# Kernel optimization log

Measured on AMD Instinct MI355X. Metric: run time of the kernel, lower is better.

## Reference

```python
import jax, jax.numpy as jnp
import numpy as np


def silu(x):
    return x * jax.nn.sigmoid(x)


def setup_inputs() -> dict:
    key = jax.random.key(0)
    ks = jax.random.split(key, 12)
    B, S, Dm = 2, 2048, 768
    I, N, R, K = 1536, 16, 48, 4
    s = 0.02
    return {
        "input_states": jax.random.normal(ks[0], (B, S, Dm), jnp.float32),
        "in_proj_w": jax.random.normal(ks[1], (2 * I, Dm), jnp.float32) * s,
        "conv_w": jax.random.normal(ks[2], (I, 1, K), jnp.float32) * s,
        "conv_b": jax.random.normal(ks[3], (I,), jnp.float32) * s,
        "x_proj_w": jax.random.normal(ks[4], (R + 2 * N, I), jnp.float32) * s,
        "dt_proj_w": jax.random.normal(ks[5], (I, R), jnp.float32) * s,
        "dt_proj_b": jax.random.normal(ks[6], (I,), jnp.float32) * s,
        "A_log": jax.random.normal(ks[7], (I, N), jnp.float32) * 0.5,
        "D": jax.random.normal(ks[8], (I,), jnp.float32) * s,
        "out_proj_w": jax.random.normal(ks[9], (Dm, I), jnp.float32) * s,
        "alpha": jax.random.uniform(ks[10], (I,), jnp.float32),
        "feature_gating": jax.random.uniform(ks[11], (I,), jnp.float32),
    }


def reference(input_states, in_proj_w, conv_w, conv_b, x_proj_w,
              dt_proj_w, dt_proj_b, A_log, D, out_proj_w,
              alpha, feature_gating):
    Bsz, S, _ = input_states.shape
    I, N = A_log.shape
    R = dt_proj_w.shape[1]
    K = conv_w.shape[-1]

    # in_proj (no bias), chunk into hidden / gate, each [B, I, S]
    proj = jnp.einsum('bsd,ed->bse', input_states, in_proj_w)  # [B, S, 2I]
    hidden, gate = jnp.split(proj.transpose(0, 2, 1), 2, axis=1)

    # causal depthwise conv1d + SiLU
    h = jax.lax.conv_general_dilated(
        hidden, conv_w, window_strides=(1,), padding=[(K - 1, 0)],
        dimension_numbers=('NCH', 'OIH', 'NCH'), feature_group_count=I)
    h = silu(h + conv_b[None, :, None])  # [B, I, S]

    # x_proj -> time_step, B, C
    ssm_p = jnp.einsum('bis,ei->bse', h, x_proj_w)  # [B, S, R+2N]
    ts, Bm, Cm = jnp.split(ssm_p, [R, R + N], axis=-1)

    dt = jax.nn.softplus(jnp.einsum('bsr,ir->bsi', ts, dt_proj_w) + dt_proj_b)
    dt = dt.transpose(0, 2, 1)                       # [B, I, S]
    dt = dt.at[:, :, -1].multiply(alpha[None, :])    # alpha scales last step

    A = -jnp.exp(A_log.astype(jnp.float32))          # [I, N]
    dA = jnp.exp(A[None, :, None, :] * dt[:, :, :, None])       # [B, I, S, N]
    dBu = dt[:, :, :, None] * Bm[:, None, :, :] * h[:, :, :, None]  # [B, I, S, N]

    def step(state, xs):
        dA_t, dBu_t, C_t = xs
        state = dA_t * state + dBu_t                 # [B, I, N]
        y = jnp.einsum('bin,bn->bi', state, C_t)
        return state, y

    init = jnp.zeros((Bsz, I, N), input_states.dtype)
    _, ys = jax.lax.scan(
        step, init,
        (dA.transpose(2, 0, 1, 3), dBu.transpose(2, 0, 1, 3), Cm.transpose(1, 0, 2)))
    y = ys.transpose(1, 2, 0)                        # [B, I, S]

    y = (y + h * D[None, :, None]) * silu(gate)
    y = y.at[:, :, -1].multiply(feature_gating[None, :])
    return jnp.einsum('bis,di->bsd', y, out_proj_w)  # [B, S, Dm]
```

## Files before the change

### kernel.cpp

```cpp
#include <hip/hip_runtime.h>
#include <math.h>


static constexpr int S_LEN  = 2048;
static constexpr int DMODEL = 768;
static constexpr int ICH    = 1536;
static constexpr int NST    = 16;
static constexpr int MROWS  = 4096;
static constexpr int NCH    = 64;
static constexpr int CHS    = 32;
static constexpr int CSTR   = 2 * ICH * NST;

typedef _Float16 f16;
typedef f16 f16x8 __attribute__((ext_vector_type(8)));
typedef f16 f16x4 __attribute__((ext_vector_type(4)));
typedef f16 f16x2 __attribute__((ext_vector_type(2)));
typedef float f32x4 __attribute__((ext_vector_type(4)));

#if __has_builtin(__builtin_amdgcn_exp2f)
#define EXP2F(x) __builtin_amdgcn_exp2f(x)
#else
#define EXP2F(x) exp2f(x)
#endif

typedef __attribute__((address_space(3))) void lds_void;
typedef const __attribute__((address_space(1))) void glb_void;

__device__ __forceinline__ void glds16(f16* l, const f16* g) {
    __builtin_amdgcn_global_load_lds((glb_void*)g, (lds_void*)l, 16, 0, 0);
}

__device__ __forceinline__ float silu_f(float x) {
    return x / (1.0f + __expf(-x));
}

__global__ __launch_bounds__(256) void cvt3(
    const float* __restrict__ s0, f16* __restrict__ d0, int n0,
    const float* __restrict__ s1, f16* __restrict__ d1, int n1,
    const float* __restrict__ s2, f16* __restrict__ d2)
{
    int i = (blockIdx.x * 256 + threadIdx.x) * 4;
    const float* s; f16* d;
    if (i < n0)            { s = s0 + i;            d = d0 + i; }
    else if (i < n0 + n1)  { s = s1 + (i - n0);     d = d1 + (i - n0); }
    else                   { s = s2 + (i - n0 - n1); d = d2 + (i - n0 - n1); }
    float4 v = *(const float4*)s;
    f16x4 o = { (f16)v.x, (f16)v.y, (f16)v.z, (f16)v.w };
    *(f16x4*)d = o;
}

__global__ __launch_bounds__(256) void k1m(
    const f16* __restrict__ Xh,
    const f16* __restrict__ Wh,
    f16* __restrict__ hidden,
    f16* __restrict__ sgate)
{
    __shared__ __align__(16) f16 As[2][128 * 32];
    __shared__ __align__(16) f16 Bs[2][64 * 32];
    const int tid = threadIdx.x;
    const int lane = tid & 63, wave = tid >> 6;
    const int quad = lane >> 4, l16 = lane & 15;
    const int wm = wave & 1, wn = wave >> 1;
    const int m0 = blockIdx.x * 128, n0 = blockIdx.y * 64;
    const int l_row = lane >> 2, l_c8 = (lane & 3) * 8;

    const f16* Ag = Xh + (size_t)(m0 + wave * 16 + l_row) * 768 + l_c8;
    const f16* Bg = Wh + (size_t)(n0 + wave * 16 + l_row) * 768 + l_c8;
    const int aLo = (wave * 16) * 32, aHi = (64 + wave * 16) * 32;
    const int bOff = (wave * 16) * 32;

#define K1_STAGE(buf, kk)                                        \
    do {                                                         \
        glds16(&As[buf][aLo], Ag + (kk));                        \
        glds16(&As[buf][aHi], Ag + (size_t)64 * 768 + (kk));     \
        glds16(&Bs[buf][bOff], Bg + (kk));                       \
    } while (0)

#define K1_COMPUTE(buf)                                                        \
    do {                                                                       \
        f16x8 af[4], bf[2];                                                    \
        _Pragma("unroll")                                                      \
        for (int mi = 0; mi < 4; ++mi)                                         \
            af[mi] = *(const f16x8*)&As[buf][(wm * 64 + mi * 16 + l16) * 32 + quad * 8]; \
        _Pragma("unroll")                                                      \
        for (int ni = 0; ni < 2; ++ni)                                         \
            bf[ni] = *(const f16x8*)&Bs[buf][(wn * 32 + ni * 16 + l16) * 32 + quad * 8]; \
        _Pragma("unroll")                                                      \
        for (int mi = 0; mi < 4; ++mi)                                         \
            _Pragma("unroll")                                                  \
            for (int ni = 0; ni < 2; ++ni)                                     \
                acc[mi][ni] = __builtin_amdgcn_mfma_f32_16x16x32_f16(          \
                    af[mi], bf[ni], acc[mi][ni], 0, 0, 0);                     \
    } while (0)

    K1_STAGE(0, 0);
    __syncthreads();

    f32x4 acc[4][2] = {};
    for (int k0 = 0; k0 < 768; k0 += 64) {
        K1_STAGE(1, k0 + 32);
        K1_COMPUTE(0);
        __syncthreads();
        if (k0 + 64 < 768) K1_STAGE(0, k0 + 64);
        K1_COMPUTE(1);
        __syncthreads();
    }
#undef K1_STAGE
#undef K1_COMPUTE

    const bool isGate = (n0 >= ICH);
    f16* outp = isGate ? sgate : hidden;
    const int e0 = (isGate ? (n0 - ICH) : n0) + wn * 32 + l16;
    #pragma unroll
    for (int mi = 0; mi < 4; ++mi) {
        #pragma unroll
        for (int ni = 0; ni < 2; ++ni) {
            #pragma unroll
            for (int r = 0; r < 4; ++r) {
                int m = m0 + wm * 64 + mi * 16 + quad * 4 + r;
                int e = e0 + ni * 16;
                float v = acc[mi][ni][r];
                if (isGate) v = silu_f(v);
                outp[(size_t)m * ICH + e] = (f16)v;
            }
        }
    }
}

__global__ __launch_bounds__(256) void k2_conv(
    const f16* __restrict__ hidden,
    const float* __restrict__ conv_w,
    const float* __restrict__ conv_b,
    f16* __restrict__ h)
{
    int idx = blockIdx.x * 256 + threadIdx.x;
    int i4 = idx % 384;
    int m  = idx / 384;
    int s  = m & (S_LEN - 1);
    const f16* base = hidden + (size_t)m * ICH + i4 * 4;
    const int c0 = i4 * 4;
    float4 wa = *(const float4*)(conv_w + (c0 + 0) * 4);
    float4 wb = *(const float4*)(conv_w + (c0 + 1) * 4);
    float4 wc = *(const float4*)(conv_w + (c0 + 2) * 4);
    float4 wd = *(const float4*)(conv_w + (c0 + 3) * 4);
    float4 bv = *(const float4*)(conv_b + c0);
    f16x4 z = {};
    f16x4 x0 = *(const f16x4*)(base);
    f16x4 x1 = (s >= 1) ? *(const f16x4*)(base - ICH)     : z;
    f16x4 x2 = (s >= 2) ? *(const f16x4*)(base - 2 * ICH) : z;
    f16x4 x3 = (s >= 3) ? *(const f16x4*)(base - 3 * ICH) : z;
    float r0 = bv.x + wa.x * (float)x3[0] + wa.y * (float)x2[0] + wa.z * (float)x1[0] + wa.w * (float)x0[0];
    float r1 = bv.y + wb.x * (float)x3[1] + wb.y * (float)x2[1] + wb.z * (float)x1[1] + wb.w * (float)x0[1];
    float r2 = bv.z + wc.x * (float)x3[2] + wc.y * (float)x2[2] + wc.z * (float)x1[2] + wc.w * (float)x0[2];
    float r3 = bv.w + wd.x * (float)x3[3] + wd.y * (float)x2[3] + wd.z * (float)x1[3] + wd.w * (float)x0[3];
    f16x4 r = { (f16)silu_f(r0), (f16)silu_f(r1), (f16)silu_f(r2), (f16)silu_f(r3) };
    *(f16x4*)(h + (size_t)m * ICH + i4 * 4) = r;
}

__global__ __launch_bounds__(256) void k3m(
    const f16* __restrict__ h,
    const float* __restrict__ xw,
    float* __restrict__ ssmp)
{
    __shared__ __align__(16) f16 Ah[128 * 32];
    __shared__ __align__(16) f16 Bh[80 * 32];
    const int tid = threadIdx.x;
    const int lane = tid & 63, wave = tid >> 6;
    const int quad = lane >> 4, l16 = lane & 15;
    const int m0 = blockIdx.x * 128;
    const int kbeg = blockIdx.y * 96;
    const int l_row = lane >> 2, l_c8 = (lane & 3) * 8;

    const f16* Ag = h + (size_t)(m0 + wave * 32 + l_row) * ICH + l_c8;
    f16* As0 = Ah + (wave * 32) * 32;
    f16* As1 = Ah + (wave * 32 + 16) * 32;

    f32x4 acc[2][5] = {};
    for (int k0 = kbeg; k0 < kbeg + 96; k0 += 32) {
        __syncthreads();
        glds16(As0, Ag + k0);
        glds16(As1, Ag + (size_t)16 * ICH + k0);
        {
            int c4 = (tid & 7) * 4;
            for (int r = tid >> 3; r < 80; r += 32) {
                float4 v = *(const float4*)(xw + (size_t)r * ICH + k0 + c4);
                f16x4 o = { (f16)v.x, (f16)v.y, (f16)v.z, (f16)v.w };
                *(f16x4*)&Bh[r * 32 + c4] = o;
            }
        }
        __syncthreads();
        f16x8 af[2], bf[5];
        #pragma unroll
        for (int mi = 0; mi < 2; ++mi)
            af[mi] = *(const f16x8*)&Ah[(wave * 32 + mi * 16 + l16) * 32 + quad * 8];
        #pragma unroll
        for (int j = 0; j < 5; ++j)
            bf[j] = *(const f16x8*)&Bh[(j * 16 + l16) * 32 + quad * 8];
        #pragma unroll
        for (int mi = 0; mi < 2; ++mi)
            #pragma unroll
            for (int j = 0; j < 5; ++j)
                acc[mi][j] = __builtin_amdgcn_mfma_f32_16x16x32_f16(
                    af[mi], bf[j], acc[mi][j], 0, 0, 0);
    }
    #pragma unroll
    for (int mi = 0; mi < 2; ++mi) {
        #pragma unroll
        for (int j = 0; j < 5; ++j) {
            #pragma unroll
            for (int r = 0; r < 4; ++r) {
                int m = m0 + wave * 32 + mi * 16 + quad * 4 + r;
                atomicAdd(ssmp + (size_t)m * 80 + j * 16 + l16, acc[mi][j][r]);
            }
        }
    }
}

__global__ __launch_bounds__(256) void k4m(
    const float* __restrict__ ssmp,
    const float* __restrict__ dtw,
    const float* __restrict__ dtb,
    const float* __restrict__ alpha,
    f16* __restrict__ dt)
{
    __shared__ __align__(16) f16 As[128 * 72];
    __shared__ __align__(16) f16 Bs[128 * 72];
    const int tid = threadIdx.x;
    const int lane = tid & 63, wave = tid >> 6;
    const int quad = lane >> 4, l16 = lane & 15;
    const int wm = wave & 1, wn = wave >> 1;
    const int m0 = blockIdx.x * 128, n0 = blockIdx.y * 128;
    const int srow = tid >> 1;
    const int shalf = tid & 1;

    {
        const float* sa = ssmp + (size_t)(m0 + srow) * 80 + shalf * 24;
        const float* sb = dtw + (size_t)(n0 + srow) * 48 + shalf * 24;
        f16* da = &As[srow * 72 + shalf * 24];
        f16* db = &Bs[srow * 72 + shalf * 24];
        #pragma unroll
        for (int j = 0; j < 6; ++j) {
            float4 va = *(const float4*)(sa + 4 * j);
            float4 vb = *(const float4*)(sb + 4 * j);
            f16x4 oa = { (f16)va.x, (f16)va.y, (f16)va.z, (f16)va.w };
            f16x4 ob = { (f16)vb.x, (f16)vb.y, (f16)vb.z, (f16)vb.w };
            *(f16x4*)(da + 4 * j) = oa;
            *(f16x4*)(db + 4 * j) = ob;
        }
        if (shalf) {
            f16x8 z = {};
            *(f16x8*)&As[srow * 72 + 48] = z;
            *(f16x8*)&As[srow * 72 + 56] = z;
            *(f16x8*)&Bs[srow * 72 + 48] = z;
            *(f16x8*)&Bs[srow * 72 + 56] = z;
        }
    }
    __syncthreads();

    f32x4 acc[4][4] = {};
    #pragma unroll
    for (int ks = 0; ks < 2; ++ks) {
        f16x8 af[4], bf[4];
        #pragma unroll
        for (int mi = 0; mi < 4; ++mi)
            af[mi] = *(const f16x8*)&As[(wm * 64 + mi * 16 + l16) * 72 + ks * 32 + quad * 8];
        #pragma unroll
        for (int ni = 0; ni < 4; ++ni)
            bf[ni] = *(const f16x8*)&Bs[(wn * 64 + ni * 16 + l16) * 72 + ks * 32 + quad * 8];
        #pragma unroll
        for (int mi = 0; mi < 4; ++mi)
            #pragma unroll
            for (int ni = 0; ni < 4; ++ni)
                acc[mi][ni] = __builtin_amdgcn_mfma_f32_16x16x32_f16(
                    af[mi], bf[ni], acc[mi][ni], 0, 0, 0);
    }

    #pragma unroll
    for (int ni = 0; ni < 4; ++ni) {
        int e = n0 + wn * 64 + ni * 16 + l16;
        float bias = dtb[e];
        float al = alpha[e];
        #pragma unroll
        for (int mi = 0; mi < 4; ++mi) {
            #pragma unroll
            for (int r = 0; r < 4; ++r) {
                int m = m0 + wm * 64 + mi * 16 + quad * 4 + r;
                float x = acc[mi][ni][r] + bias;
                float sp = (x > 20.0f) ? x : __logf(1.0f + __expf(x));
                if ((m & (S_LEN - 1)) == S_LEN - 1) sp *= al;
                dt[(size_t)m * ICH + e] = (f16)sp;
            }
        }
    }
}

__global__ __launch_bounds__(256) void k5a_chunk(
    const f16* __restrict__ dt,
    const f16* __restrict__ h,
    const float* __restrict__ ssmp,
    const float* __restrict__ A_log,
    float* __restrict__ PArr,
    float* __restrict__ SfArr)
{
    __shared__ float dts[CHS * 64];
    __shared__ float hs[CHS * 64];
    __shared__ float Bc[CHS][16];
    const int tid = threadIdx.x;
    const int n4 = tid & 3;
    const int il = tid >> 2;
    const int i0 = blockIdx.x * 64;
    const int i = i0 + il;
    const int c = blockIdx.y;
    const int b = blockIdx.z;
    const int s0 = c * CHS;
    const size_t row0 = (size_t)(b * S_LEN + s0) * ICH + i0;

    #pragma unroll
    for (int k = 0; k < (CHS * 64) / 512; ++k) {
        int idx = (tid + k * 256) * 2;
        size_t g_off = row0 + (size_t)(idx >> 6) * ICH + (idx & 63);
        f16x2 dv = *(const f16x2*)(dt + g_off);
        f16x2 hv = *(const f16x2*)(h + g_off);
        dts[idx] = (float)dv[0]; dts[idx + 1] = (float)dv[1];
        hs[idx]  = (float)hv[0]; hs[idx + 1]  = (float)hv[1];
    }
    if (tid < CHS * 4) {
        int t = tid >> 2, q = tid & 3;
        *(float4*)&Bc[t][q * 4] =
            *(const float4*)(ssmp + (size_t)(b * S_LEN + s0 + t) * 80 + 48 + q * 4);
    }

    const float L2E = 1.44269504088896f;
    float4 alv = *(const float4*)(A_log + i * NST + n4 * 4);
    float A[4] = { -__expf(alv.x) * L2E, -__expf(alv.y) * L2E,
                   -__expf(alv.z) * L2E, -__expf(alv.w) * L2E };
    float st[4] = {};
    float cdt = 0.f;
    __syncthreads();
    #pragma unroll 4
    for (int t = 0; t < CHS; ++t) {
        float dtv = dts[t * 64 + il];
        float hv  = hs[t * 64 + il];
        float4 Bv = *(const float4*)&Bc[t][n4 * 4];
        cdt += dtv;
        float x = dtv * hv;
        #pragma unroll
        for (int j = 0; j < 4; ++j) {
            float dA = EXP2F(A[j] * dtv);
            st[j] = fmaf(dA, st[j], x * (&Bv.x)[j]);
        }
    }
    size_t base = (size_t)c * CSTR + (size_t)(b * ICH + i) * NST + n4 * 4;
    float4 Pv = { EXP2F(A[0] * cdt), EXP2F(A[1] * cdt),
                  EXP2F(A[2] * cdt), EXP2F(A[3] * cdt) };
    float4 Sv = { st[0], st[1], st[2], st[3] };
    *(float4*)(PArr + base)  = Pv;
    *(float4*)(SfArr + base) = Sv;
}

__global__ __launch_bounds__(256) void k5b_carry(
    const float* PArr,
    const float* __restrict__ SfArr,
    float* CIn)
{
    int idx = blockIdx.x * 256 + threadIdx.x;
    float p[NCH], s[NCH];
    #pragma unroll
    for (int c = 0; c < NCH; ++c) {
        size_t a = (size_t)c * CSTR + idx;
        p[c] = PArr[a];
        s[c] = SfArr[a];
    }
    float carry = 0.f;
    #pragma unroll
    for (int c = 0; c < NCH; ++c) {
        CIn[(size_t)c * CSTR + idx] = carry;
        carry = fmaf(p[c], carry, s[c]);
    }
}

__global__ __launch_bounds__(256) void k5c_emit(
    const f16* __restrict__ dt,
    const f16* __restrict__ h,
    const f16* __restrict__ sgate,
    const float* __restrict__ ssmp,
    const float* __restrict__ A_log,
    const float* __restrict__ Dp,
    const float* __restrict__ fg,
    const float* __restrict__ CIn,
    f16* __restrict__ yh)
{
    __shared__ float dts[CHS * 64];
    __shared__ float hs[CHS * 64];
    __shared__ float gs[CHS * 64];
    __shared__ float BC[CHS][32];
    const int tid = threadIdx.x;
    const int n4 = tid & 3;
    const int il = tid >> 2;
    const int i0 = blockIdx.x * 64;
    const int i = i0 + il;
    const int c = blockIdx.y;
    const int b = blockIdx.z;
    const int s0 = c * CHS;
    const size_t row0 = (size_t)(b * S_LEN + s0) * ICH + i0;

    #pragma unroll
    for (int k = 0; k < (CHS * 64) / 512; ++k) {
        int idx = (tid + k * 256) * 2;
        size_t g_off = row0 + (size_t)(idx >> 6) * ICH + (idx & 63);
        f16x2 dv = *(const f16x2*)(dt + g_off);
        f16x2 v = *(const f16x2*)(h + g_off);
        f16x2 w = *(const f16x2*)(sgate + g_off);
        dts[idx] = (float)dv[0]; dts[idx + 1] = (float)dv[1];
        hs[idx] = (float)v[0]; hs[idx + 1] = (float)v[1];
        gs[idx] = (float)w[0]; gs[idx + 1] = (float)w[1];
    }
    {
        int t = tid >> 3, q = tid & 7;
        *(float4*)&BC[t][q * 4] =
            *(const float4*)(ssmp + (size_t)(b * S_LEN + s0 + t) * 80 + 48 + q * 4);
    }

    const float L2E = 1.44269504088896f;
    float4 alv = *(const float4*)(A_log + i * NST + n4 * 4);
    float A[4] = { -__expf(alv.x) * L2E, -__expf(alv.y) * L2E,
                   -__expf(alv.z) * L2E, -__expf(alv.w) * L2E };
    const float Dv = Dp[i];
    const float fgv = fg[i];
    float4 civ = *(const float4*)(CIn + (size_t)c * CSTR + (size_t)(b * ICH + i) * NST + n4 * 4);
    float st[4] = { civ.x, civ.y, civ.z, civ.w };
    f16* yout = yh + row0 + il;
    const bool last_chunk = (c == NCH - 1);
    __syncthreads();
    #pragma unroll 4
    for (int t = 0; t < CHS; ++t) {
        float dtv = dts[t * 64 + il];
        float hv  = hs[t * 64 + il];
        float4 Bv = *(const float4*)&BC[t][n4 * 4];
        float4 Cv = *(const float4*)&BC[t][16 + n4 * 4];
        float x = dtv * hv;
        float yp = 0.f;
        #pragma unroll
        for (int j = 0; j < 4; ++j) {
            float dA = EXP2F(A[j] * dtv);
            st[j] = fmaf(dA, st[j], x * (&Bv.x)[j]);
            yp = fmaf(st[j], (&Cv.x)[j], yp);
        }
        yp += __shfl_xor(yp, 1, 4);
        yp += __shfl_xor(yp, 2, 4);
        if (n4 == 0) {
            float yv = fmaf(hv, Dv, yp) * gs[t * 64 + il];
            if (last_chunk && t == CHS - 1) yv *= fgv;
            yout[(size_t)t * ICH] = (f16)yv;
        }
    }
}

__global__ __launch_bounds__(256) void k6m(
    const f16* __restrict__ Yh,
    const f16* __restrict__ Wh,
    float* __restrict__ out)
{
    __shared__ __align__(16) f16 As[2][128 * 32];
    __shared__ __align__(16) f16 Bs[2][64 * 32];
    const int tid = threadIdx.x;
    const int lane = tid & 63, wave = tid >> 6;
    const int quad = lane >> 4, l16 = lane & 15;
    const int wm = wave & 1, wn = wave >> 1;
    const int m0 = blockIdx.x * 128, n0 = blockIdx.y * 64;
    const int l_row = lane >> 2, l_c8 = (lane & 3) * 8;

    const f16* Ag = Yh + (size_t)(m0 + wave * 16 + l_row) * ICH + l_c8;
    const f16* Bg = Wh + (size_t)(n0 + wave * 16 + l_row) * ICH + l_c8;
    const int aLo = (wave * 16) * 32, aHi = (64 + wave * 16) * 32;
    const int bOff = (wave * 16) * 32;

#define K6_STAGE(buf, kk)                                        \
    do {                                                         \
        glds16(&As[buf][aLo], Ag + (kk));                        \
        glds16(&As[buf][aHi], Ag + (size_t)64 * ICH + (kk));     \
        glds16(&Bs[buf][bOff], Bg + (kk));                       \
    } while (0)

#define K6_COMPUTE(buf)                                                        \
    do {                                                                       \
        f16x8 af[4], bf[2];                                                    \
        _Pragma("unroll")                                                      \
        for (int mi = 0; mi < 4; ++mi)                                         \
            af[mi] = *(const f16x8*)&As[buf][(wm * 64 + mi * 16 + l16) * 32 + quad * 8]; \
        _Pragma("unroll")                                                      \
        for (int ni = 0; ni < 2; ++ni)                                         \
            bf[ni] = *(const f16x8*)&Bs[buf][(wn * 32 + ni * 16 + l16) * 32 + quad * 8]; \
        _Pragma("unroll")                                                      \
        for (int mi = 0; mi < 4; ++mi)                                         \
            _Pragma("unroll")                                                  \
            for (int ni = 0; ni < 2; ++ni)                                     \
                acc[mi][ni] = __builtin_amdgcn_mfma_f32_16x16x32_f16(          \
                    af[mi], bf[ni], acc[mi][ni], 0, 0, 0);                     \
    } while (0)

    K6_STAGE(0, 0);
    __syncthreads();

    f32x4 acc[4][2] = {};
    for (int k0 = 0; k0 < ICH; k0 += 64) {
        K6_STAGE(1, k0 + 32);
        K6_COMPUTE(0);
        __syncthreads();
        if (k0 + 64 < ICH) K6_STAGE(0, k0 + 64);
        K6_COMPUTE(1);
        __syncthreads();
    }
#undef K6_STAGE
#undef K6_COMPUTE

    #pragma unroll
    for (int mi = 0; mi < 4; ++mi) {
        #pragma unroll
        for (int ni = 0; ni < 2; ++ni) {
            #pragma unroll
            for (int r = 0; r < 4; ++r) {
                int m = m0 + wm * 64 + mi * 16 + quad * 4 + r;
                int d = n0 + wn * 32 + ni * 16 + l16;
                out[(size_t)m * DMODEL + d] = acc[mi][ni][r];
            }
        }
    }
}

extern "C" void kernel_launch(void* const* d_in, const int* in_sizes, int n_in,
                              void* d_out, int out_size, void* d_ws, size_t ws_size,
                              hipStream_t stream) {
    const float* X     = (const float*)d_in[0];
    const float* W1    = (const float*)d_in[1];
    const float* CW    = (const float*)d_in[2];
    const float* CB    = (const float*)d_in[3];
    const float* XW    = (const float*)d_in[4];
    const float* DTW   = (const float*)d_in[5];
    const float* DTB   = (const float*)d_in[6];
    const float* ALOG  = (const float*)d_in[7];
    const float* DD    = (const float*)d_in[8];
    const float* OW    = (const float*)d_in[9];
    const float* ALPHA = (const float*)d_in[10];
    const float* FG    = (const float*)d_in[11];
    float* out = (float*)d_out;

    const size_t NBI = (size_t)MROWS * ICH;
    f16* hidden_h = (f16*)d_ws;
    f16* sgate_h  = hidden_h + NBI;
    f16* h_h      = sgate_h + NBI;
    f16* dt_h     = h_h + NBI;
    float* ssmp   = (float*)(dt_h + NBI);
    f16* Xh       = (f16*)(ssmp + (size_t)MROWS * 80);
    f16* W1h      = Xh + (size_t)MROWS * DMODEL;
    f16* OWh      = W1h + (size_t)2 * ICH * DMODEL;
    float* SfA    = (float*)(OWh + (size_t)DMODEL * ICH);
    float* PArr = (float*)hidden_h;
    float* CIn  = PArr;
    f16* yh     = (f16*)SfA;

    const int nX = MROWS * DMODEL, nW1 = 2 * ICH * DMODEL, nOW = DMODEL * ICH;
    hipMemsetAsync(ssmp, 0, (size_t)MROWS * 80 * sizeof(float), stream);
    cvt3<<<dim3((nX + nW1 + nOW) / 1024), 256, 0, stream>>>(X, Xh, nX, W1, W1h, nW1, OW, OWh);
    k1m<<<dim3(32, 48), 256, 0, stream>>>(Xh, W1h, hidden_h, sgate_h);
    k2_conv<<<dim3((MROWS * 384) / 256), 256, 0, stream>>>(hidden_h, CW, CB, h_h);
    k3m<<<dim3(32, 16), 256, 0, stream>>>(h_h, XW, ssmp);
    k4m<<<dim3(32, 12), 256, 0, stream>>>(ssmp, DTW, DTB, ALPHA, dt_h);
    k5a_chunk<<<dim3(24, NCH, 2), 256, 0, stream>>>(dt_h, h_h, ssmp, ALOG, PArr, SfA);
    k5b_carry<<<dim3(192), 256, 0, stream>>>(PArr, SfA, CIn);
    k5c_emit<<<dim3(24, NCH, 2), 256, 0, stream>>>(dt_h, h_h, sgate_h, ssmp, ALOG, DD, FG, CIn, yh);
    k6m<<<dim3(32, 12), 256, 0, stream>>>(yh, OWh, out);
}
```

Before: 248.7 us.

## Fuse conv into x_proj GEMM, split-K out_proj with atomics and inline weight cast

Folds the causal depthwise conv plus SiLU into the x_proj GEMM's A-tile load, so hidden is read once and h is written from there, and the separate conv kernel goes away. The out_proj GEMM becomes split-K across four z-slices that accumulate with atomicAdd into an output that is zeroed inside the carry kernel. It also reads fp32 out_proj weights directly and converts them to fp16 while staging to LDS, which removes that conversion from the cast kernel. In exchange it adds redundant neighbour loads in the fused GEMM, atomic traffic on the output, and order-dependent float summation.

```diff
diff --git a/kernel.cpp b/kernel.cpp
--- a/kernel.cpp
+++ b/kernel.cpp
@@ -34,16 +34,14 @@
     return x / (1.0f + __expf(-x));
 }
 
-__global__ __launch_bounds__(256) void cvt3(
+__global__ __launch_bounds__(256) void cvt2(
     const float* __restrict__ s0, f16* __restrict__ d0, int n0,
-    const float* __restrict__ s1, f16* __restrict__ d1, int n1,
-    const float* __restrict__ s2, f16* __restrict__ d2)
+    const float* __restrict__ s1, f16* __restrict__ d1)
 {
     int i = (blockIdx.x * 256 + threadIdx.x) * 4;
     const float* s; f16* d;
-    if (i < n0)            { s = s0 + i;            d = d0 + i; }
-    else if (i < n0 + n1)  { s = s1 + (i - n0);     d = d1 + (i - n0); }
-    else                   { s = s2 + (i - n0 - n1); d = d2 + (i - n0 - n1); }
+    if (i < n0)            { s = s0 + i;        d = d0 + i; }
+    else                   { s = s1 + (i - n0); d = d1 + (i - n0); }
     float4 v = *(const float4*)s;
     f16x4 o = { (f16)v.x, (f16)v.y, (f16)v.z, (f16)v.w };
     *(f16x4*)d = o;
@@ -127,59 +125,57 @@
     }
 }
 
-__global__ __launch_bounds__(256) void k2_conv(
+__global__ __launch_bounds__(256) void k3m(
     const f16* __restrict__ hidden,
     const float* __restrict__ conv_w,
     const float* __restrict__ conv_b,
-    f16* __restrict__ h)
-{
-    int idx = blockIdx.x * 256 + threadIdx.x;
-    int i4 = idx % 384;
-    int m  = idx / 384;
-    int s  = m & (S_LEN - 1);
-    const f16* base = hidden + (size_t)m * ICH + i4 * 4;
-    const int c0 = i4 * 4;
-    float4 wa = *(const float4*)(conv_w + (c0 + 0) * 4);
-    float4 wb = *(const float4*)(conv_w + (c0 + 1) * 4);
-    float4 wc = *(const float4*)(conv_w + (c0 + 2) * 4);
-    float4 wd = *(const float4*)(conv_w + (c0 + 3) * 4);
-    float4 bv = *(const float4*)(conv_b + c0);
-    f16x4 z = {};
-    f16x4 x0 = *(const f16x4*)(base);
-    f16x4 x1 = (s >= 1) ? *(const f16x4*)(base - ICH)     : z;
-    f16x4 x2 = (s >= 2) ? *(const f16x4*)(base - 2 * ICH) : z;
-    f16x4 x3 = (s >= 3) ? *(const f16x4*)(base - 3 * ICH) : z;
-    float r0 = bv.x + wa.x * (float)x3[0] + wa.y * (float)x2[0] + wa.z * (float)x1[0] + wa.w * (float)x0[0];
-    float r1 = bv.y + wb.x * (float)x3[1] + wb.y * (float)x2[1] + wb.z * (float)x1[1] + wb.w * (float)x0[1];
-    float r2 = bv.z + wc.x * (float)x3[2] + wc.y * (float)x2[2] + wc.z * (float)x1[2] + wc.w * (float)x0[2];
-    float r3 = bv.w + wd.x * (float)x3[3] + wd.y * (float)x2[3] + wd.z * (float)x1[3] + wd.w * (float)x0[3];
-    f16x4 r = { (f16)silu_f(r0), (f16)silu_f(r1), (f16)silu_f(r2), (f16)silu_f(r3) };
-    *(f16x4*)(h + (size_t)m * ICH + i4 * 4) = r;
-}
-
-__global__ __launch_bounds__(256) void k3m(
-    const f16* __restrict__ h,
     const float* __restrict__ xw,
+    f16* __restrict__ h,
     float* __restrict__ ssmp)
 {
     __shared__ __align__(16) f16 Ah[128 * 32];
     __shared__ __align__(16) f16 Bh[80 * 32];
+    __shared__ float4 cwv[96];
+    __shared__ float  cbv[96];
     const int tid = threadIdx.x;
     const int lane = tid & 63, wave = tid >> 6;
     const int quad = lane >> 4, l16 = lane & 15;
     const int m0 = blockIdx.x * 128;
     const int kbeg = blockIdx.y * 96;
-    const int l_row = lane >> 2, l_c8 = (lane & 3) * 8;
-
-    const f16* Ag = h + (size_t)(m0 + wave * 32 + l_row) * ICH + l_c8;
-    f16* As0 = Ah + (wave * 32) * 32;
-    f16* As1 = Ah + (wave * 32 + 16) * 32;
+
+    if (tid < 96) {
+        cwv[tid] = *(const float4*)(conv_w + (size_t)(kbeg + tid) * 4);
+        cbv[tid] = conv_b[kbeg + tid];
+    }
 
     f32x4 acc[2][5] = {};
     for (int k0 = kbeg; k0 < kbeg + 96; k0 += 32) {
         __syncthreads();
-        glds16(As0, Ag + k0);
-        glds16(As1, Ag + (size_t)16 * ICH + k0);
+        #pragma unroll
+        for (int it = 0; it < 2; ++it) {
+            int slot = tid + it * 256;
+            int r_ = slot >> 2, c_ = (slot & 3) * 8;
+            int gm = m0 + r_, c = k0 + c_;
+            int s = gm & (S_LEN - 1);
+            const f16* bp = hidden + (size_t)gm * ICH + c;
+            f16x8 x0 = *(const f16x8*)bp;
+            f16x8 x1 = *(const f16x8*)(bp - (s >= 1 ? ICH : 0));
+            f16x8 x2 = *(const f16x8*)(bp - (s >= 2 ? 2 * ICH : 0));
+            f16x8 x3 = *(const f16x8*)(bp - (s >= 3 ? 3 * ICH : 0));
+            f16x8 o;
+            #pragma unroll
+            for (int j = 0; j < 8; ++j) {
+                int ci = (k0 - kbeg) + c_ + j;
+                float4 w = cwv[ci];
+                float v1 = (s >= 1) ? (float)x1[j] : 0.f;
+                float v2 = (s >= 2) ? (float)x2[j] : 0.f;
+                float v3 = (s >= 3) ? (float)x3[j] : 0.f;
+                float r = cbv[ci] + w.x * v3 + w.y * v2 + w.z * v1 + w.w * (float)x0[j];
+                o[j] = (f16)silu_f(r);
+            }
+            *(f16x8*)&Ah[r_ * 32 + c_] = o;
+            *(f16x8*)(h + (size_t)gm * ICH + c) = o;
+        }
         {
             int c4 = (tid & 7) * 4;
             for (int r = tid >> 3; r < 80; r += 32) {
@@ -361,9 +357,15 @@
 __global__ __launch_bounds__(256) void k5b_carry(
     const float* PArr,
     const float* __restrict__ SfArr,
-    float* CIn)
+    float* CIn,
+    float* __restrict__ outz)
 {
     int idx = blockIdx.x * 256 + threadIdx.x;
+    #pragma unroll
+    for (int j = 0; j < 16; ++j) {
+        float4 z = {};
+        *(float4*)(outz + (size_t)j * 196608 + (size_t)idx * 4) = z;
+    }
     float p[NCH], s[NCH];
     #pragma unroll
     for (int c = 0; c < NCH; ++c) {
@@ -458,8 +460,8 @@
 
 __global__ __launch_bounds__(256) void k6m(
     const f16* __restrict__ Yh,
-    const f16* __restrict__ Wh,
-    float* __restrict__ out)
+    const float* __restrict__ OWf,
+    float* out)
 {
     __shared__ __align__(16) f16 As[2][128 * 32];
     __shared__ __align__(16) f16 Bs[2][64 * 32];
@@ -468,18 +470,32 @@
     const int quad = lane >> 4, l16 = lane & 15;
     const int wm = wave & 1, wn = wave >> 1;
     const int m0 = blockIdx.x * 128, n0 = blockIdx.y * 64;
+    const int kbeg = blockIdx.z * 384;
     const int l_row = lane >> 2, l_c8 = (lane & 3) * 8;
 
     const f16* Ag = Yh + (size_t)(m0 + wave * 16 + l_row) * ICH + l_c8;
-    const f16* Bg = Wh + (size_t)(n0 + wave * 16 + l_row) * ICH + l_c8;
     const int aLo = (wave * 16) * 32, aHi = (64 + wave * 16) * 32;
-    const int bOff = (wave * 16) * 32;
-
-#define K6_STAGE(buf, kk)                                        \
+    const int brow = tid >> 2, bc8 = (tid & 3) * 8;
+    const float* Bgf = OWf + (size_t)(n0 + brow) * ICH + bc8;
+    float4 vb0, vb1;
+
+#define K6_STAGEA(buf, kk)                                       \
     do {                                                         \
         glds16(&As[buf][aLo], Ag + (kk));                        \
         glds16(&As[buf][aHi], Ag + (size_t)64 * ICH + (kk));     \
-        glds16(&Bs[buf][bOff], Bg + (kk));                       \
+    } while (0)
+
+#define K6_LOADB(kk)                                             \
+    do {                                                         \
+        vb0 = *(const float4*)(Bgf + (kk));                      \
+        vb1 = *(const float4*)(Bgf + (kk) + 4);                  \
+    } while (0)
+
+#define K6_WRITEB(buf)                                                         \
+    do {                                                                       \
+        f16x8 o = { (f16)vb0.x, (f16)vb0.y, (f16)vb0.z, (f16)vb0.w,            \
+                    (f16)vb1.x, (f16)vb1.y, (f16)vb1.z, (f16)vb1.w };          \
+        *(f16x8*)&Bs[buf][brow * 32 + bc8] = o;                                \
     } while (0)
 
 #define K6_COMPUTE(buf)                                                        \
@@ -499,19 +515,28 @@
                     af[mi], bf[ni], acc[mi][ni], 0, 0, 0);                     \
     } while (0)
 
-    K6_STAGE(0, 0);
+    K6_STAGEA(0, kbeg);
+    K6_LOADB(kbeg);
+    K6_WRITEB(0);
     __syncthreads();
 
     f32x4 acc[4][2] = {};
-    for (int k0 = 0; k0 < ICH; k0 += 64) {
-        K6_STAGE(1, k0 + 32);
-        K6_COMPUTE(0);
-        __syncthreads();
-        if (k0 + 64 < ICH) K6_STAGE(0, k0 + 64);
-        K6_COMPUTE(1);
-        __syncthreads();
-    }
-#undef K6_STAGE
+    int cur = 0;
+    for (int ks = 0; ks < 12; ++ks) {
+        if (ks < 11) {
+            K6_STAGEA(cur ^ 1, kbeg + (ks + 1) * 32);
+            K6_LOADB(kbeg + (ks + 1) * 32);
+        }
+        K6_COMPUTE(cur);
+        if (ks < 11) {
+            K6_WRITEB(cur ^ 1);
+            __syncthreads();
+        }
+        cur ^= 1;
+    }
+#undef K6_STAGEA
+#undef K6_LOADB
+#undef K6_WRITEB
 #undef K6_COMPUTE
 
     #pragma unroll
@@ -522,7 +547,7 @@
             for (int r = 0; r < 4; ++r) {
                 int m = m0 + wm * 64 + mi * 16 + quad * 4 + r;
                 int d = n0 + wn * 32 + ni * 16 + l16;
-                out[(size_t)m * DMODEL + d] = acc[mi][ni][r];
+                atomicAdd(out + (size_t)m * DMODEL + d, acc[mi][ni][r]);
             }
         }
     }
@@ -553,21 +578,19 @@
     float* ssmp   = (float*)(dt_h + NBI);
     f16* Xh       = (f16*)(ssmp + (size_t)MROWS * 80);
     f16* W1h      = Xh + (size_t)MROWS * DMODEL;
-    f16* OWh      = W1h + (size_t)2 * ICH * DMODEL;
-    float* SfA    = (float*)(OWh + (size_t)DMODEL * ICH);
+    float* SfA    = (float*)(W1h + (size_t)2 * ICH * DMODEL);
     float* PArr = (float*)hidden_h;
     float* CIn  = PArr;
     f16* yh     = (f16*)SfA;
 
-    const int nX = MROWS * DMODEL, nW1 = 2 * ICH * DMODEL, nOW = DMODEL * ICH;
+    const int nX = MROWS * DMODEL, nW1 = 2 * ICH * DMODEL;
     hipMemsetAsync(ssmp, 0, (size_t)MROWS * 80 * sizeof(float), stream);
-    cvt3<<<dim3((nX + nW1 + nOW) / 1024), 256, 0, stream>>>(X, Xh, nX, W1, W1h, nW1, OW, OWh);
+    cvt2<<<dim3((nX + nW1) / 1024), 256, 0, stream>>>(X, Xh, nX, W1, W1h);
     k1m<<<dim3(32, 48), 256, 0, stream>>>(Xh, W1h, hidden_h, sgate_h);
-    k2_conv<<<dim3((MROWS * 384) / 256), 256, 0, stream>>>(hidden_h, CW, CB, h_h);
-    k3m<<<dim3(32, 16), 256, 0, stream>>>(h_h, XW, ssmp);
+    k3m<<<dim3(32, 16), 256, 0, stream>>>(hidden_h, CW, CB, XW, h_h, ssmp);
     k4m<<<dim3(32, 12), 256, 0, stream>>>(ssmp, DTW, DTB, ALPHA, dt_h);
     k5a_chunk<<<dim3(24, NCH, 2), 256, 0, stream>>>(dt_h, h_h, ssmp, ALOG, PArr, SfA);
-    k5b_carry<<<dim3(192), 256, 0, stream>>>(PArr, SfA, CIn);
+    k5b_carry<<<dim3(192), 256, 0, stream>>>(PArr, SfA, CIn, out);
     k5c_emit<<<dim3(24, NCH, 2), 256, 0, stream>>>(dt_h, h_h, sgate_h, ssmp, ALOG, DD, FG, CIn, yh);
-    k6m<<<dim3(32, 12), 256, 0, stream>>>(yh, OWh, out);
-}
+    k6m<<<dim3(32, 12, 4), 256, 0, stream>>>(yh, OW, out);
+}
```

Result: slower. 273.0 us (+9.8%).

## Fuse causal conv+SiLU into x_proj GEMM and shrink out_proj M-tile

Applied to the files above, without the earlier changes.

Drops the standalone conv kernel. The x_proj GEMM now loads the raw hidden tile, computes the 4-tap causal depthwise conv plus SiLU in registers, and writes the result both to shared memory for the MFMA and to global h for the later scan kernels. This removes one launch and one full read of h. The out_proj GEMM tile is cut from 128 to 64 rows, doubling the grid from 384 to 768 blocks to improve CU occupancy, at the cost of more reloads of the weight operand.

```diff
diff --git a/kernel.cpp b/kernel.cpp
--- a/kernel.cpp
+++ b/kernel.cpp
@@ -127,59 +127,57 @@
     }
 }
 
-__global__ __launch_bounds__(256) void k2_conv(
+__global__ __launch_bounds__(256) void k3m(
     const f16* __restrict__ hidden,
     const float* __restrict__ conv_w,
     const float* __restrict__ conv_b,
-    f16* __restrict__ h)
-{
-    int idx = blockIdx.x * 256 + threadIdx.x;
-    int i4 = idx % 384;
-    int m  = idx / 384;
-    int s  = m & (S_LEN - 1);
-    const f16* base = hidden + (size_t)m * ICH + i4 * 4;
-    const int c0 = i4 * 4;
-    float4 wa = *(const float4*)(conv_w + (c0 + 0) * 4);
-    float4 wb = *(const float4*)(conv_w + (c0 + 1) * 4);
-    float4 wc = *(const float4*)(conv_w + (c0 + 2) * 4);
-    float4 wd = *(const float4*)(conv_w + (c0 + 3) * 4);
-    float4 bv = *(const float4*)(conv_b + c0);
-    f16x4 z = {};
-    f16x4 x0 = *(const f16x4*)(base);
-    f16x4 x1 = (s >= 1) ? *(const f16x4*)(base - ICH)     : z;
-    f16x4 x2 = (s >= 2) ? *(const f16x4*)(base - 2 * ICH) : z;
-    f16x4 x3 = (s >= 3) ? *(const f16x4*)(base - 3 * ICH) : z;
-    float r0 = bv.x + wa.x * (float)x3[0] + wa.y * (float)x2[0] + wa.z * (float)x1[0] + wa.w * (float)x0[0];
-    float r1 = bv.y + wb.x * (float)x3[1] + wb.y * (float)x2[1] + wb.z * (float)x1[1] + wb.w * (float)x0[1];
-    float r2 = bv.z + wc.x * (float)x3[2] + wc.y * (float)x2[2] + wc.z * (float)x1[2] + wc.w * (float)x0[2];
-    float r3 = bv.w + wd.x * (float)x3[3] + wd.y * (float)x2[3] + wd.z * (float)x1[3] + wd.w * (float)x0[3];
-    f16x4 r = { (f16)silu_f(r0), (f16)silu_f(r1), (f16)silu_f(r2), (f16)silu_f(r3) };
-    *(f16x4*)(h + (size_t)m * ICH + i4 * 4) = r;
-}
-
-__global__ __launch_bounds__(256) void k3m(
-    const f16* __restrict__ h,
     const float* __restrict__ xw,
+    f16* __restrict__ h,
     float* __restrict__ ssmp)
 {
     __shared__ __align__(16) f16 Ah[128 * 32];
     __shared__ __align__(16) f16 Bh[80 * 32];
+    __shared__ float4 cwv[96];
+    __shared__ float  cbv[96];
     const int tid = threadIdx.x;
     const int lane = tid & 63, wave = tid >> 6;
     const int quad = lane >> 4, l16 = lane & 15;
     const int m0 = blockIdx.x * 128;
     const int kbeg = blockIdx.y * 96;
-    const int l_row = lane >> 2, l_c8 = (lane & 3) * 8;
-
-    const f16* Ag = h + (size_t)(m0 + wave * 32 + l_row) * ICH + l_c8;
-    f16* As0 = Ah + (wave * 32) * 32;
-    f16* As1 = Ah + (wave * 32 + 16) * 32;
+
+    if (tid < 96) {
+        cwv[tid] = *(const float4*)(conv_w + (size_t)(kbeg + tid) * 4);
+        cbv[tid] = conv_b[kbeg + tid];
+    }
 
     f32x4 acc[2][5] = {};
     for (int k0 = kbeg; k0 < kbeg + 96; k0 += 32) {
         __syncthreads();
-        glds16(As0, Ag + k0);
-        glds16(As1, Ag + (size_t)16 * ICH + k0);
+        #pragma unroll
+        for (int it = 0; it < 2; ++it) {
+            int slot = tid + it * 256;
+            int r_ = slot >> 2, c_ = (slot & 3) * 8;
+            int gm = m0 + r_, c = k0 + c_;
+            int s = gm & (S_LEN - 1);
+            const f16* bp = hidden + (size_t)gm * ICH + c;
+            f16x8 x0 = *(const f16x8*)bp;
+            f16x8 x1 = *(const f16x8*)(bp - (s >= 1 ? ICH : 0));
+            f16x8 x2 = *(const f16x8*)(bp - (s >= 2 ? 2 * ICH : 0));
+            f16x8 x3 = *(const f16x8*)(bp - (s >= 3 ? 3 * ICH : 0));
+            f16x8 o;
+            #pragma unroll
+            for (int j = 0; j < 8; ++j) {
+                int ci = (k0 - kbeg) + c_ + j;
+                float4 w = cwv[ci];
+                float v1 = (s >= 1) ? (float)x1[j] : 0.f;
+                float v2 = (s >= 2) ? (float)x2[j] : 0.f;
+                float v3 = (s >= 3) ? (float)x3[j] : 0.f;
+                float r = cbv[ci] + w.x * v3 + w.y * v2 + w.z * v1 + w.w * (float)x0[j];
+                o[j] = (f16)silu_f(r);
+            }
+            *(f16x8*)&Ah[r_ * 32 + c_] = o;
+            *(f16x8*)(h + (size_t)gm * ICH + c) = o;
+        }
         {
             int c4 = (tid & 7) * 4;
             for (int r = tid >> 3; r < 80; r += 32) {
@@ -461,38 +459,36 @@
     const f16* __restrict__ Wh,
     float* __restrict__ out)
 {
-    __shared__ __align__(16) f16 As[2][128 * 32];
+    __shared__ __align__(16) f16 As[2][64 * 32];
     __shared__ __align__(16) f16 Bs[2][64 * 32];
     const int tid = threadIdx.x;
     const int lane = tid & 63, wave = tid >> 6;
     const int quad = lane >> 4, l16 = lane & 15;
     const int wm = wave & 1, wn = wave >> 1;
-    const int m0 = blockIdx.x * 128, n0 = blockIdx.y * 64;
+    const int m0 = blockIdx.x * 64, n0 = blockIdx.y * 64;
     const int l_row = lane >> 2, l_c8 = (lane & 3) * 8;
 
     const f16* Ag = Yh + (size_t)(m0 + wave * 16 + l_row) * ICH + l_c8;
     const f16* Bg = Wh + (size_t)(n0 + wave * 16 + l_row) * ICH + l_c8;
-    const int aLo = (wave * 16) * 32, aHi = (64 + wave * 16) * 32;
-    const int bOff = (wave * 16) * 32;
+    const int aOff = (wave * 16) * 32;
 
 #define K6_STAGE(buf, kk)                                        \
     do {                                                         \
-        glds16(&As[buf][aLo], Ag + (kk));                        \
-        glds16(&As[buf][aHi], Ag + (size_t)64 * ICH + (kk));     \
-        glds16(&Bs[buf][bOff], Bg + (kk));                       \
+        glds16(&As[buf][aOff], Ag + (kk));                       \
+        glds16(&Bs[buf][aOff], Bg + (kk));                       \
     } while (0)
 
 #define K6_COMPUTE(buf)                                                        \
     do {                                                                       \
-        f16x8 af[4], bf[2];                                                    \
+        f16x8 af[2], bf[2];                                                    \
         _Pragma("unroll")                                                      \
-        for (int mi = 0; mi < 4; ++mi)                                         \
-            af[mi] = *(const f16x8*)&As[buf][(wm * 64 + mi * 16 + l16) * 32 + quad * 8]; \
+        for (int mi = 0; mi < 2; ++mi)                                         \
+            af[mi] = *(const f16x8*)&As[buf][(wm * 32 + mi * 16 + l16) * 32 + quad * 8]; \
         _Pragma("unroll")                                                      \
         for (int ni = 0; ni < 2; ++ni)                                         \
             bf[ni] = *(const f16x8*)&Bs[buf][(wn * 32 + ni * 16 + l16) * 32 + quad * 8]; \
         _Pragma("unroll")                                                      \
-        for (int mi = 0; mi < 4; ++mi)                                         \
+        for (int mi = 0; mi < 2; ++mi)                                         \
             _Pragma("unroll")                                                  \
             for (int ni = 0; ni < 2; ++ni)                                     \
                 acc[mi][ni] = __builtin_amdgcn_mfma_f32_16x16x32_f16(          \
@@ -502,7 +498,7 @@
     K6_STAGE(0, 0);
     __syncthreads();
 
-    f32x4 acc[4][2] = {};
+    f32x4 acc[2][2] = {};
     for (int k0 = 0; k0 < ICH; k0 += 64) {
         K6_STAGE(1, k0 + 32);
         K6_COMPUTE(0);
@@ -515,12 +511,12 @@
 #undef K6_COMPUTE
 
     #pragma unroll
-    for (int mi = 0; mi < 4; ++mi) {
+    for (int mi = 0; mi < 2; ++mi) {
         #pragma unroll
         for (int ni = 0; ni < 2; ++ni) {
             #pragma unroll
             for (int r = 0; r < 4; ++r) {
-                int m = m0 + wm * 64 + mi * 16 + quad * 4 + r;
+                int m = m0 + wm * 32 + mi * 16 + quad * 4 + r;
                 int d = n0 + wn * 32 + ni * 16 + l16;
                 out[(size_t)m * DMODEL + d] = acc[mi][ni][r];
             }
@@ -563,11 +559,10 @@
     hipMemsetAsync(ssmp, 0, (size_t)MROWS * 80 * sizeof(float), stream);
     cvt3<<<dim3((nX + nW1 + nOW) / 1024), 256, 0, stream>>>(X, Xh, nX, W1, W1h, nW1, OW, OWh);
     k1m<<<dim3(32, 48), 256, 0, stream>>>(Xh, W1h, hidden_h, sgate_h);
-    k2_conv<<<dim3((MROWS * 384) / 256), 256, 0, stream>>>(hidden_h, CW, CB, h_h);
-    k3m<<<dim3(32, 16), 256, 0, stream>>>(h_h, XW, ssmp);
+    k3m<<<dim3(32, 16), 256, 0, stream>>>(hidden_h, CW, CB, XW, h_h, ssmp);
     k4m<<<dim3(32, 12), 256, 0, stream>>>(ssmp, DTW, DTB, ALPHA, dt_h);
     k5a_chunk<<<dim3(24, NCH, 2), 256, 0, stream>>>(dt_h, h_h, ssmp, ALOG, PArr, SfA);
     k5b_carry<<<dim3(192), 256, 0, stream>>>(PArr, SfA, CIn);
     k5c_emit<<<dim3(24, NCH, 2), 256, 0, stream>>>(dt_h, h_h, sgate_h, ssmp, ALOG, DD, FG, CIn, yh);
-    k6m<<<dim3(32, 12), 256, 0, stream>>>(yh, OWh, out);
-}
+    k6m<<<dim3(64, 12), 256, 0, stream>>>(yh, OWh, out);
+}
```

New measurement: 243.1 us. 1.02x faster.
